# Optimization experiments

Hardware: AMD Instinct MI355X
Metric: run time of the kernel (lower is better)

Reference implementation:

```python
import jax, jax.numpy as jnp
import numpy as np

N, E = 50000, 800000
D_IN, H, D_OUT = 100, 128, 40
N_MID = 2  # num_layers(5) - 3
EPS = 1e-5


def setup_inputs() -> dict:
    key = jax.random.key(0)
    ks = iter(jax.random.split(key, 40))
    rn = lambda shape, s=0.05: jax.random.normal(next(ks), shape, dtype=jnp.float32) * s
    inp = {
        "x": jax.random.normal(next(ks), (N, D_IN), dtype=jnp.float32),
        "edge_index": jax.random.randint(next(ks), (2, E), 0, N, dtype=jnp.int64),
        "percent": 70,
        "ricci_curvature": jax.random.normal(next(ks), (E,), dtype=jnp.float32),
        # GCNConv weights/biases
        "W1": rn((D_IN, H)), "b1": jnp.zeros((H,), jnp.float32),
        "W2": rn((D_IN + H, H)), "b2": jnp.zeros((H,), jnp.float32),
        "Wm": rn((N_MID, 2 * H, H)), "bm": jnp.zeros((N_MID, H), jnp.float32),
        "Wo": rn((2 * H, D_OUT)), "bo": jnp.zeros((D_OUT,), jnp.float32),
    }
    # BatchNorm1d params + running stats (eval mode)
    def bn_params(dim, lead=()):
        return (jnp.ones(lead + (dim,), jnp.float32),            # gamma
                jnp.zeros(lead + (dim,), jnp.float32),           # beta
                rn(lead + (dim,), 0.1),                          # running mean
                1.0 + 0.1 * jax.random.uniform(next(ks), lead + (dim,), dtype=jnp.float32))  # running var
    inp["bn1_g"], inp["bn1_b"], inp["bn1_m"], inp["bn1_v"] = bn_params(D_IN)
    inp["bn2_g"], inp["bn2_b"], inp["bn2_m"], inp["bn2_v"] = bn_params(D_IN + H)
    inp["bnm_g"], inp["bnm_b"], inp["bnm_m"], inp["bnm_v"] = bn_params(2 * H, (N_MID,))
    inp["bno_g"], inp["bno_b"], inp["bno_m"], inp["bno_v"] = bn_params(2 * H)
    return inp


def reference(x, edge_index, percent, ricci_curvature,
              W1, b1, W2, b2, Wm, bm, Wo, bo,
              bn1_g, bn1_b, bn1_m, bn1_v,
              bn2_g, bn2_b, bn2_m, bn2_v,
              bnm_g, bnm_b, bnm_m, bnm_v,
              bno_g, bno_b, bno_m, bno_v):
    # Eval mode: no sampling / dynamic edge weights, dropout = identity,
    # BN uses running stats. GCNConv = PyG: add self-loops, sym-norm D^-1/2 A D^-1/2.
    n = x.shape[0]
    loop = jnp.arange(n)
    src = jnp.concatenate([edge_index[0], loop])  # [E+N]
    dst = jnp.concatenate([edge_index[1], loop])
    deg = jnp.zeros((n,), x.dtype).at[dst].add(1.0)  # >=1 thanks to self-loops
    dis = jax.lax.rsqrt(deg)
    norm = (dis[src] * dis[dst])[:, None]  # [E+N, 1]

    def gcn(h, W, b):
        hw = h @ W  # [N, out]
        agg = jnp.zeros((n, W.shape[1]), h.dtype).at[dst].add(hw[src] * norm)
        return agg + b

    def bn(h, g, bta, m, v):
        return (h - m) * (g * jax.lax.rsqrt(v + EPS)) + bta

    res = []
    x_in = x
    h = jax.nn.relu(gcn(bn(x, bn1_g, bn1_b, bn1_m, bn1_v), W1, b1))
    res.append(h)
    h = jnp.concatenate([h, x_in], axis=1)  # [N, H+D_IN]
    h = jax.nn.relu(gcn(bn(h, bn2_g, bn2_b, bn2_m, bn2_v), W2, b2))
    res.append(h)
    h = jnp.concatenate([h, res[-2]], axis=1)  # [N, 2H]
    for i in range(Wm.shape[0]):
        hi = jax.nn.relu(gcn(bn(h, bnm_g[i], bnm_b[i], bnm_m[i], bnm_v[i]), Wm[i], bm[i]))
        res.append(hi)
        h = jnp.concatenate([hi, res[-2]], axis=1)
    out = gcn(bn(h, bno_g, bno_b, bno_m, bno_v), Wo, bo)
    return (out, *res)
```

## Files before the change

### kernel.cpp

```cpp
#include <hip/hip_runtime.h>
#include <hip/hip_bf16.h>
#include <cstdint>
#include <cstddef>

#define BN_EPS 1e-5f
typedef long long ll;
using bf16x8 = __attribute__((ext_vector_type(8))) short;
using f32x4  = __attribute__((ext_vector_type(4))) float;

__device__ __forceinline__ unsigned short f2bf(float f) {
    union { float f; unsigned u; } c; c.f = f;
    unsigned u = c.u;
    u += 0x7fff + ((u >> 16) & 1);
    return (unsigned short)(u >> 16);
}
__device__ __forceinline__ float bf2f(unsigned h) {
    union { unsigned u; float f; } c; c.u = h << 16;
    return c.f;
}
__device__ __forceinline__ void addbf(float* a, uint2 v) {
    a[0] += bf2f(v.x & 0xffffu); a[1] += bf2f(v.x >> 16);
    a[2] += bf2f(v.y & 0xffffu); a[3] += bf2f(v.y >> 16);
}
__device__ __forceinline__ float4 bf4_to_f4(uint2 v) {
    return make_float4(bf2f(v.x & 0xffffu), bf2f(v.x >> 16),
                       bf2f(v.y & 0xffffu), bf2f(v.y >> 16));
}

__global__ __launch_bounds__(1024) void detect_kernel(const int* ei32, int* flag) {
    __shared__ int any;
    if (threadIdx.x == 0) any = 0;
    __syncthreads();
    for (int i = threadIdx.x; i < 2048; i += 1024) {
        if (ei32[2 * i + 1] != 0) any = 1;
    }
    __syncthreads();
    if (threadIdx.x == 0) *flag = (any == 0) ? 1 : 0;
}

__global__ void init_kernel(int* deg, int* cursor, int N) {
    int i = blockIdx.x * 256 + threadIdx.x;
    if (i < N) { deg[i] = 1; cursor[i] = 0; }
}

__global__ void count_kernel(const void* ei, int E, int* deg, const int* flag) {
    int e = blockIdx.x * 256 + threadIdx.x;
    if (e >= E) return;
    int d = (*flag) ? (int)((const ll*)ei)[(size_t)E + e]
                    : ((const int*)ei)[(size_t)E + e];
    atomicAdd(&deg[d], 1);
}

__global__ __launch_bounds__(1024) void scanA_kernel(const int* deg, int* row_ptr,
                                                     int* bsum, float* dis, int N) {
    __shared__ int wsum[16];
    int i = blockIdx.x * 1024 + threadIdx.x;
    int lane = threadIdx.x & 63, wid = threadIdx.x >> 6;
    int dv = (i < N) ? deg[i] : 1;
    if (i < N) dis[i] = rsqrtf((float)dv);
    int v = (i < N) ? (dv - 1) : 0;
    int s = v;
#pragma unroll
    for (int o = 1; o < 64; o <<= 1) { int t = __shfl_up(s, o); if (lane >= o) s += t; }
    if (lane == 63) wsum[wid] = s;
    __syncthreads();
    if (threadIdx.x < 16) {
        int w = wsum[threadIdx.x];
        int ws_ = w;
#pragma unroll
        for (int o = 1; o < 16; o <<= 1) { int t = __shfl_up(ws_, o); if ((int)threadIdx.x >= o) ws_ += t; }
        wsum[threadIdx.x] = ws_ - w;
    }
    __syncthreads();
    s += wsum[wid];
    if (i < N) row_ptr[i + 1] = s;
    if (threadIdx.x == 1023) bsum[blockIdx.x] = s;
}

__global__ void scanB_kernel(int* bsum, int nb) {
    int lane = threadIdx.x;
    int v = (lane < nb) ? bsum[lane] : 0;
    int s = v;
#pragma unroll
    for (int o = 1; o < 64; o <<= 1) { int t = __shfl_up(s, o); if (lane >= o) s += t; }
    if (lane < nb) bsum[lane] = s - v;
}

__global__ __launch_bounds__(1024) void scanC_kernel(int* row_ptr, const int* bsum, int N) {
    int i = blockIdx.x * 1024 + threadIdx.x;
    if (i < N) row_ptr[i + 1] += bsum[blockIdx.x];
    if (i == 0) row_ptr[0] = 0;
}

__global__ void fill_kernel(const void* ei, int E, const int* row_ptr,
                            int* cursor, int* csr, const int* flag) {
    int e = blockIdx.x * 256 + threadIdx.x;
    if (e >= E) return;
    int s, d;
    if (*flag) { const ll* p = (const ll*)ei; s = (int)p[e]; d = (int)p[(size_t)E + e]; }
    else       { const int* p = (const int*)ei; s = p[e]; d = p[(size_t)E + e]; }
    int pos = atomicAdd(&cursor[d], 1);
    csr[row_ptr[d] + pos] = s;
}

struct LayerP {
    const float *W, *g, *b, *m, *v;
    int K, Dout, ncb, boff;
};
struct LayerPs { LayerP l[5]; };

__global__ __launch_bounds__(256) void fold_b_all(LayerPs P,
                                                  unsigned short* __restrict__ Bhi,
                                                  unsigned short* __restrict__ Blo) {
    const LayerP& L = P.l[blockIdx.y];
    int nkc = (L.K + 63) >> 6 << 1;
    int total = nkc * L.ncb * 512;
    int idx = blockIdx.x * 256 + threadIdx.x;
    if (idx >= total) return;
    int i = idx & 7;
    int lane = (idx >> 3) & 63;
    int cb = (idx >> 9) % L.ncb;
    int kc = (idx >> 9) / L.ncb;
    int k = kc * 32 + (lane >> 4) * 8 + i;
    int col = cb * 16 + (lane & 15);
    float val = 0.f;
    if (k < L.K && col < L.Dout) {
        float s = L.g[k] * rsqrtf(L.v[k] + BN_EPS);
        val = L.W[k * L.Dout + col] * s;
    }
    unsigned short h = f2bf(val);
    Bhi[L.boff + idx] = h;
    Blo[L.boff + idx] = f2bf(val - bf2f(h));
}

__global__ __launch_bounds__(256) void fold_c_all(LayerPs P, float* __restrict__ cvecA) {
    const LayerP& L = P.l[blockIdx.y];
    int wid = threadIdx.x >> 6, lane = threadIdx.x & 63;
    int col = blockIdx.x * 4 + wid;
    float acc = 0.f;
    if (col < L.Dout) {
        for (int k = lane; k < L.K; k += 64) {
            float s = L.g[k] * rsqrtf(L.v[k] + BN_EPS);
            acc += (L.b[k] - L.m[k] * s) * L.W[k * L.Dout + col];
        }
    }
#pragma unroll
    for (int o = 32; o >= 1; o >>= 1) acc += __shfl_xor(acc, o);
    if (lane == 0 && col < 128) cvecA[128 * blockIdx.y + col] = (col < L.Dout) ? acc : 0.f;
}

template <int NCB, bool B1, bool B2>
__global__ __launch_bounds__(256, 3) void gemm_mix_kernel(
    const void* __restrict__ X1, int K1, int ld1,
    const void* __restrict__ X2, int ld2,
    const unsigned short* __restrict__ Bhi, const unsigned short* __restrict__ Blo,
    const float* __restrict__ cvec, const float* __restrict__ dis,
    unsigned short* __restrict__ outp, int ldH, int Dout, int K, int kc_lo, int N)
{
    __shared__ float Xs[64 * 64];
    const int tid = threadIdx.x;
    const int w = tid >> 6, lane = tid & 63;
    const int lr = lane & 15, lg = lane >> 4;
    const int brow = blockIdx.x * 64;
    const int nkt = (K + 63) >> 6;

    f32x4 acc[NCB];
#pragma unroll
    for (int cb = 0; cb < NCB; ++cb) {
        float cv = cvec[cb * 16 + lr];
        f32x4 iv = {cv, cv, cv, cv};
        acc[cb] = iv;
    }

    for (int kt = 0; kt < nkt; ++kt) {
        const int k0 = kt * 64;
#pragma unroll
        for (int p = 0; p < 4; ++p) {
            int fidx = (p * 256 + tid) * 4;
            int r = fidx >> 6;
            int c = fidx & 63;
            int grow = brow + r;
            int k = k0 + c;
            float4 val = make_float4(0.f, 0.f, 0.f, 0.f);
            if (grow < N) {
                if (k < K1) {
                    if (B1) val = bf4_to_f4(*(const uint2*)((const unsigned short*)X1 + (size_t)grow * ld1 + k));
                    else    val = *(const float4*)((const float*)X1 + (size_t)grow * ld1 + k);
                } else if (k < K) {
                    int kk = k - K1;
                    if (B2) val = bf4_to_f4(*(const uint2*)((const unsigned short*)X2 + (size_t)grow * ld2 + kk));
                    else    val = *(const float4*)((const float*)X2 + (size_t)grow * ld2 + kk);
                }
            }
            *(float4*)((char*)Xs + r * 256 + ((c * 4) ^ ((r & 7) << 4))) = val;
        }
        __syncthreads();

        const int r = w * 16 + lr;
        const char* base = (const char*)Xs + r * 256;
        const int swz = (r & 7) << 4;
#pragma unroll
        for (int ks = 0; ks < 2; ++ks) {
            const int kcg = kt * 2 + ks;
            const bool need_lo = (kcg >= kc_lo);
            int cb0 = ks * 128 + lg * 32;
            float4 v0 = *(const float4*)(base + (cb0 ^ swz));
            float4 v1 = *(const float4*)(base + ((cb0 + 16) ^ swz));
            float xv[8] = {v0.x, v0.y, v0.z, v0.w, v1.x, v1.y, v1.z, v1.w};
            bf16x8 ahi, alo;
#pragma unroll
            for (int i = 0; i < 8; ++i) {
                unsigned short h = f2bf(xv[i]);
                ahi[i] = (short)h;
                alo[i] = need_lo ? (short)f2bf(xv[i] - bf2f(h)) : (short)0;
            }
            const bf16x8* bh = (const bf16x8*)Bhi + (size_t)kcg * NCB * 64;
            const bf16x8* bl = (const bf16x8*)Blo + (size_t)kcg * NCB * 64;
#pragma unroll
            for (int cb = 0; cb < NCB; ++cb) {
                bf16x8 bhf = bh[cb * 64 + lane];
                bf16x8 blf = bl[cb * 64 + lane];
                acc[cb] = __builtin_amdgcn_mfma_f32_16x16x32_bf16(ahi, bhf, acc[cb], 0, 0, 0);
                acc[cb] = __builtin_amdgcn_mfma_f32_16x16x32_bf16(ahi, blf, acc[cb], 0, 0, 0);
                if (need_lo)
                    acc[cb] = __builtin_amdgcn_mfma_f32_16x16x32_bf16(alo, bhf, acc[cb], 0, 0, 0);
            }
        }
        __syncthreads();
    }

#pragma unroll
    for (int r = 0; r < 4; ++r) {
        int grow = brow + w * 16 + lg * 4 + r;
        if (grow >= N) continue;
        float d = dis[grow];
#pragma unroll
        for (int cb = 0; cb < NCB; ++cb) {
            int col = cb * 16 + lr;
            if (col < Dout) outp[(size_t)grow * ldH + col] = f2bf(d * acc[cb][r]);
        }
    }
}

template <int NCB>
__global__ __launch_bounds__(256, 4) void gemm_bf_kernel(
    const unsigned short* __restrict__ X1, int K1, int ld1,
    const unsigned short* __restrict__ X2, int ld2,
    const unsigned short* __restrict__ Bhi, const unsigned short* __restrict__ Blo,
    const float* __restrict__ cvec, const float* __restrict__ dis,
    unsigned short* __restrict__ outp, int ldH, int Dout, int K, int N)
{
    __shared__ unsigned short Xs[64 * 64];
    const int tid = threadIdx.x;
    const int w = tid >> 6, lane = tid & 63;
    const int lr = lane & 15, lg = lane >> 4;
    const int brow = blockIdx.x * 64;
    const int nkt = (K + 63) >> 6;

    f32x4 acc[NCB];
#pragma unroll
    for (int cb = 0; cb < NCB; ++cb) {
        float cv = cvec[cb * 16 + lr];
        f32x4 iv = {cv, cv, cv, cv};
        acc[cb] = iv;
    }

    for (int kt = 0; kt < nkt; ++kt) {
        const int k0 = kt * 64;
#pragma unroll
        for (int p = 0; p < 2; ++p) {
            int idx = p * 256 + tid;
            int r = idx >> 3;
            int sl = idx & 7;
            int grow = brow + r;
            int k = k0 + sl * 8;
            uint4 raw = make_uint4(0, 0, 0, 0);
            if (grow < N) {
                if (k < K1)      raw = *(const uint4*)(X1 + (size_t)grow * ld1 + k);
                else if (k < K)  raw = *(const uint4*)(X2 + (size_t)grow * ld2 + (k - K1));
            }
            *(uint4*)((char*)Xs + r * 128 + ((sl * 16) ^ ((r & 7) << 4))) = raw;
        }
        __syncthreads();

        const int r = w * 16 + lr;
        const char* base = (const char*)Xs + r * 128;
        const int swz = (r & 7) << 4;
        bf16x8 a0 = *(const bf16x8*)(base + ((lg * 16) ^ swz));
        bf16x8 a1 = *(const bf16x8*)(base + ((64 + lg * 16) ^ swz));
#pragma unroll
        for (int ks = 0; ks < 2; ++ks) {
            const int kcg = kt * 2 + ks;
            const bf16x8 af = ks ? a1 : a0;
            const bf16x8* bh = (const bf16x8*)Bhi + (size_t)kcg * NCB * 64;
            const bf16x8* bl = (const bf16x8*)Blo + (size_t)kcg * NCB * 64;
#pragma unroll
            for (int cb = 0; cb < NCB; ++cb) {
                bf16x8 bhf = bh[cb * 64 + lane];
                bf16x8 blf = bl[cb * 64 + lane];
                acc[cb] = __builtin_amdgcn_mfma_f32_16x16x32_bf16(af, bhf, acc[cb], 0, 0, 0);
                acc[cb] = __builtin_amdgcn_mfma_f32_16x16x32_bf16(af, blf, acc[cb], 0, 0, 0);
            }
        }
        __syncthreads();
    }

#pragma unroll
    for (int r = 0; r < 4; ++r) {
        int grow = brow + w * 16 + lg * 4 + r;
        if (grow >= N) continue;
        float d = dis[grow];
#pragma unroll
        for (int cb = 0; cb < NCB; ++cb) {
            int col = cb * 16 + lr;
            if (col < Dout) outp[(size_t)grow * ldH + col] = f2bf(d * acc[cb][r]);
        }
    }
}

template <bool RELU>
__global__ __launch_bounds__(256) void agg128b_kernel(
    const unsigned short* __restrict__ hwb,
    const int* __restrict__ row_ptr, const int* __restrict__ csr,
    const float* __restrict__ dis, const float* __restrict__ bias,
    float* __restrict__ outp, unsigned short* __restrict__ hbout, int N)
{
    int wid = threadIdx.x >> 6, lane = threadIdx.x & 63;
    int node = blockIdx.x * 4 + wid;
    if (node >= N) return;
    const int half = lane >> 5, q = lane & 31;
    const uint2* hw2 = (const uint2*)hwb;
    float a[4] = {0.f, 0.f, 0.f, 0.f};
    float b4[4] = {0.f, 0.f, 0.f, 0.f};
    if (half == 0) addbf(a, hw2[(size_t)node * 32 + q]);
    int beg = row_ptr[node], end = row_ptr[node + 1];
    for (int base = beg; base < end; base += 64) {
        int idx = base + lane;
        int j = (idx < end) ? csr[idx] : 0;
        int cnt = end - base; if (cnt > 64) cnt = 64;
        int fullp = cnt >> 1;
        int t = 0;
        for (; t + 4 <= fullp; t += 4) {
            int ja = __shfl(j, 2 * t     + half);
            int jb = __shfl(j, 2 * t + 2 + half);
            int jc = __shfl(j, 2 * t + 4 + half);
            int jd = __shfl(j, 2 * t + 6 + half);
            uint2 va = hw2[(size_t)ja * 32 + q];
            uint2 vb = hw2[(size_t)jb * 32 + q];
            uint2 vc = hw2[(size_t)jc * 32 + q];
            uint2 vd = hw2[(size_t)jd * 32 + q];
            addbf(a, va); addbf(b4, vb); addbf(a, vc); addbf(b4, vd);
        }
        for (; t < fullp; ++t) {
            int ja = __shfl(j, 2 * t + half);
            uint2 va = hw2[(size_t)ja * 32 + q];
            addbf(a, va);
        }
        if (cnt & 1) {
            int ja = __shfl(j, cnt - 1);
            if (half == 0) { uint2 va = hw2[(size_t)ja * 32 + q]; addbf(a, va); }
        }
    }
#pragma unroll
    for (int c = 0; c < 4; ++c) {
        a[c] += b4[c];
        a[c] += __shfl_xor(a[c], 32);
    }
    if (half == 0) {
        float d = dis[node];
        float4 bv = ((const float4*)bias)[q];
        float4 o;
        o.x = fmaf(d, a[0], bv.x);
        o.y = fmaf(d, a[1], bv.y);
        o.z = fmaf(d, a[2], bv.z);
        o.w = fmaf(d, a[3], bv.w);
        if (RELU) {
            o.x = fmaxf(o.x, 0.f); o.y = fmaxf(o.y, 0.f);
            o.z = fmaxf(o.z, 0.f); o.w = fmaxf(o.w, 0.f);
        }
        ((float4*)outp)[(size_t)node * 32 + q] = o;
        uint2 pk;
        pk.x = (unsigned)f2bf(o.x) | ((unsigned)f2bf(o.y) << 16);
        pk.y = (unsigned)f2bf(o.z) | ((unsigned)f2bf(o.w) << 16);
        ((uint2*)hbout)[(size_t)node * 32 + q] = pk;
    }
}

__global__ __launch_bounds__(256) void agg40b_kernel(
    const unsigned short* __restrict__ hwb,
    const int* __restrict__ row_ptr, const int* __restrict__ csr,
    const float* __restrict__ dis, const float* __restrict__ bias,
    float* __restrict__ outp, int N)
{
    int wid = threadIdx.x >> 6, lane = threadIdx.x & 63;
    int node = blockIdx.x * 4 + wid;
    if (node >= N) return;
    const int half = lane >> 5, q = lane & 31;
    const bool act = q < 20;
    const unsigned* hw20 = (const unsigned*)hwb;
    float a0 = 0.f, a1 = 0.f, b0 = 0.f, b1 = 0.f;
    if (half == 0 && act) {
        unsigned v = hw20[(size_t)node * 20 + q];
        a0 += bf2f(v & 0xffffu); a1 += bf2f(v >> 16);
    }
    int beg = row_ptr[node], end = row_ptr[node + 1];
    for (int base = beg; base < end; base += 64) {
        int idx = base + lane;
        int j = (idx < end) ? csr[idx] : 0;
        int cnt = end - base; if (cnt > 64) cnt = 64;
        int fullp = cnt >> 1;
        int t = 0;
        for (; t + 4 <= fullp; t += 4) {
            int ja = __shfl(j, 2 * t     + half);
            int jb = __shfl(j, 2 * t + 2 + half);
            int jc = __shfl(j, 2 * t + 4 + half);
            int jd = __shfl(j, 2 * t + 6 + half);
            if (act) {
                unsigned va = hw20[(size_t)ja * 20 + q];
                unsigned vb = hw20[(size_t)jb * 20 + q];
                unsigned vc = hw20[(size_t)jc * 20 + q];
                unsigned vd = hw20[(size_t)jd * 20 + q];
                a0 += bf2f(va & 0xffffu); a1 += bf2f(va >> 16);
                b0 += bf2f(vb & 0xffffu); b1 += bf2f(vb >> 16);
                a0 += bf2f(vc & 0xffffu); a1 += bf2f(vc >> 16);
                b0 += bf2f(vd & 0xffffu); b1 += bf2f(vd >> 16);
            }
        }
        for (; t < fullp; ++t) {
            int ja = __shfl(j, 2 * t + half);
            if (act) {
                unsigned va = hw20[(size_t)ja * 20 + q];
                a0 += bf2f(va & 0xffffu); a1 += bf2f(va >> 16);
            }
        }
        if (cnt & 1) {
            int ja = __shfl(j, cnt - 1);
            if (half == 0 && act) {
                unsigned va = hw20[(size_t)ja * 20 + q];
                a0 += bf2f(va & 0xffffu); a1 += bf2f(va >> 16);
            }
        }
    }
    a0 += b0; a1 += b1;
    a0 += __shfl_xor(a0, 32);
    a1 += __shfl_xor(a1, 32);
    if (half == 0 && act) {
        float d = dis[node];
        float2 o;
        o.x = fmaf(d, a0, bias[2 * q]);
        o.y = fmaf(d, a1, bias[2 * q + 1]);
        *(float2*)(outp + (size_t)node * 40 + 2 * q) = o;
    }
}

extern "C" void kernel_launch(void* const* d_in, const int* in_sizes, int n_in,
                              void* d_out, int out_size, void* d_ws, size_t ws_size,
                              hipStream_t stream) {
    const int N = in_sizes[0] / 100;
    const int E = in_sizes[1] / 2;

    const float* x   = (const float*)d_in[0];
    const void*  ei  = d_in[1];
    const float* W1  = (const float*)d_in[4];
    const float* b1  = (const float*)d_in[5];
    const float* W2  = (const float*)d_in[6];
    const float* b2  = (const float*)d_in[7];
    const float* Wm  = (const float*)d_in[8];
    const float* bm  = (const float*)d_in[9];
    const float* Wo  = (const float*)d_in[10];
    const float* bo  = (const float*)d_in[11];
    const float* bn1g = (const float*)d_in[12];
    const float* bn1b = (const float*)d_in[13];
    const float* bn1m = (const float*)d_in[14];
    const float* bn1v = (const float*)d_in[15];
    const float* bn2g = (const float*)d_in[16];
    const float* bn2b = (const float*)d_in[17];
    const float* bn2m = (const float*)d_in[18];
    const float* bn2v = (const float*)d_in[19];
    const float* bnmg = (const float*)d_in[20];
    const float* bnmb = (const float*)d_in[21];
    const float* bnmm = (const float*)d_in[22];
    const float* bnmv = (const float*)d_in[23];
    const float* bnog = (const float*)d_in[24];
    const float* bnob = (const float*)d_in[25];
    const float* bnom = (const float*)d_in[26];
    const float* bnov = (const float*)d_in[27];

    char* wsb = (char*)d_ws;
    size_t off = 0;
    auto alloc = [&](size_t elems) -> void* { void* p = wsb + off; off += elems * 4; return p; };
    int*   deg     = (int*)alloc(N);
    int*   cursor  = (int*)alloc(N);
    int*   row_ptr = (int*)alloc((size_t)N + 1);
    int*   bsum    = (int*)alloc(64);
    int*   flag    = (int*)alloc(1);
    off = (off + 15) & ~(size_t)15;
    float* dis  = (float*)alloc(N);
    int*   csr  = (int*)alloc(E);
    off = (off + 15) & ~(size_t)15;
    unsigned short* hwb = (unsigned short*)alloc((size_t)N * 64);
    unsigned short* hbA = (unsigned short*)alloc((size_t)N * 64);
    unsigned short* hbB = (unsigned short*)alloc((size_t)N * 64);
    unsigned short* hbC = (unsigned short*)alloc((size_t)N * 64);
    unsigned short* BhiA = (unsigned short*)alloc(63488);
    unsigned short* BloA = (unsigned short*)alloc(63488);
    float* cvecA = (float*)alloc(128 * 5);
    (void)ws_size; (void)n_in; (void)out_size;

    float* outF = (float*)d_out;
    float* h1 = outF + (size_t)N * 40;
    float* h2 = h1 + (size_t)N * 128;
    float* h3 = h2 + (size_t)N * 128;
    float* h4 = h3 + (size_t)N * 128;

    dim3 b256(256);

    LayerPs P;
    P.l[0] = {W1, bn1g, bn1b, bn1m, bn1v, 100, 128, 8, 0};
    P.l[1] = {W2, bn2g, bn2b, bn2m, bn2v, 228, 128, 8, 16384};
    P.l[2] = {Wm, bnmg, bnmb, bnmm, bnmv, 256, 128, 8, 49152};
    P.l[3] = {Wm + 256 * 128, bnmg + 256, bnmb + 256, bnmm + 256, bnmv + 256, 256, 128, 8, 81920};
    P.l[4] = {Wo, bnog, bnob, bnom, bnov, 256, 40, 3, 114688};
    fold_b_all<<<dim3(128, 5), b256, 0, stream>>>(P, BhiA, BloA);
    fold_c_all<<<dim3(32, 5), b256, 0, stream>>>(P, cvecA);

    detect_kernel<<<1, 1024, 0, stream>>>((const int*)ei, flag);
    init_kernel<<<dim3((N + 255) / 256), b256, 0, stream>>>(deg, cursor, N);
    count_kernel<<<dim3((E + 255) / 256), b256, 0, stream>>>(ei, E, deg, flag);
    int nb = (N + 1023) / 1024;
    scanA_kernel<<<dim3(nb), dim3(1024), 0, stream>>>(deg, row_ptr, bsum, dis, N);
    scanB_kernel<<<1, 64, 0, stream>>>(bsum, nb);
    scanC_kernel<<<dim3(nb), dim3(1024), 0, stream>>>(row_ptr, bsum, N);
    fill_kernel<<<dim3((E + 255) / 256), b256, 0, stream>>>(ei, E, row_ptr, cursor, csr, flag);

    int gemm_grid = (N + 63) / 64;
    int agg_grid  = (N + 3) / 4;

    auto agg128 = [&](const float* lb, float* dst, unsigned short* hbout) {
        agg128b_kernel<true><<<dim3(agg_grid), b256, 0, stream>>>(
            hwb, row_ptr, csr, dis, lb, dst, hbout, N);
    };

    gemm_mix_kernel<8, false, false><<<dim3(gemm_grid), b256, 0, stream>>>(
        x, 100, 100, nullptr, 0, BhiA + P.l[0].boff, BloA + P.l[0].boff,
        cvecA, dis, hwb, 128, 128, 100, 0, N);
    agg128(b1, h1, hbA);

    gemm_mix_kernel<8, true, false><<<dim3(gemm_grid), b256, 0, stream>>>(
        hbA, 128, 128, x, 100, BhiA + P.l[1].boff, BloA + P.l[1].boff,
        cvecA + 128, dis, hwb, 128, 128, 228, 4, N);
    agg128(b2, h2, hbB);

    gemm_bf_kernel<8><<<dim3(gemm_grid), b256, 0, stream>>>(
        hbB, 128, 128, hbA, 128, BhiA + P.l[2].boff, BloA + P.l[2].boff,
        cvecA + 256, dis, hwb, 128, 128, 256, N);
    agg128(bm, h3, hbC);

    gemm_bf_kernel<8><<<dim3(gemm_grid), b256, 0, stream>>>(
        hbC, 128, 128, hbB, 128, BhiA + P.l[3].boff, BloA + P.l[3].boff,
        cvecA + 384, dis, hwb, 128, 128, 256, N);
    agg128(bm + 128, h4, hbA);

    gemm_bf_kernel<3><<<dim3(gemm_grid), b256, 0, stream>>>(
        hbA, 128, 128, hbC, 128, BhiA + P.l[4].boff, BloA + P.l[4].boff,
        cvecA + 512, dis, hwb, 40, 40, 256, N);
    agg40b_kernel<<<dim3(agg_grid), b256, 0, stream>>>(hwb, row_ptr, csr, dis, bo, outF, N);
}
```

Baseline: 432.5 us.

## Split GEMM columns across waves, pre-convert A to bf16 in LDS, merge setup kernels

```diff
diff --git a/kernel.cpp b/kernel.cpp
--- a/kernel.cpp
+++ b/kernel.cpp
@@ -27,20 +27,18 @@
                        bf2f(v.y & 0xffffu), bf2f(v.y >> 16));
 }
 
-__global__ __launch_bounds__(1024) void detect_kernel(const int* ei32, int* flag) {
-    __shared__ int any;
-    if (threadIdx.x == 0) any = 0;
-    __syncthreads();
-    for (int i = threadIdx.x; i < 2048; i += 1024) {
-        if (ei32[2 * i + 1] != 0) any = 1;
-    }
-    __syncthreads();
-    if (threadIdx.x == 0) *flag = (any == 0) ? 1 : 0;
-}
-
-__global__ void init_kernel(int* deg, int* cursor, int N) {
+__global__ void build0_kernel(const int* ei32, int* flag, int* deg, int* cursor, int N) {
     int i = blockIdx.x * 256 + threadIdx.x;
     if (i < N) { deg[i] = 1; cursor[i] = 0; }
+    if (blockIdx.x == 0) {
+        __shared__ int any;
+        if (threadIdx.x == 0) any = 0;
+        __syncthreads();
+        for (int t = threadIdx.x; t < 2048; t += 256)
+            if (ei32[2 * t + 1] != 0) any = 1;
+        __syncthreads();
+        if (threadIdx.x == 0) *flag = (any == 0) ? 1 : 0;
+    }
 }
 
 __global__ void count_kernel(const void* ei, int E, int* deg, const int* flag) {
@@ -109,71 +107,157 @@
 };
 struct LayerPs { LayerP l[5]; };
 
-__global__ __launch_bounds__(256) void fold_b_all(LayerPs P,
-                                                  unsigned short* __restrict__ Bhi,
-                                                  unsigned short* __restrict__ Blo) {
+__global__ __launch_bounds__(256) void fold_all(LayerPs P,
+                                                unsigned short* __restrict__ Bhi,
+                                                unsigned short* __restrict__ Blo,
+                                                float* __restrict__ cvecA) {
     const LayerP& L = P.l[blockIdx.y];
-    int nkc = (L.K + 63) >> 6 << 1;
-    int total = nkc * L.ncb * 512;
-    int idx = blockIdx.x * 256 + threadIdx.x;
-    if (idx >= total) return;
-    int i = idx & 7;
-    int lane = (idx >> 3) & 63;
-    int cb = (idx >> 9) % L.ncb;
-    int kc = (idx >> 9) / L.ncb;
-    int k = kc * 32 + (lane >> 4) * 8 + i;
-    int col = cb * 16 + (lane & 15);
-    float val = 0.f;
-    if (k < L.K && col < L.Dout) {
-        float s = L.g[k] * rsqrtf(L.v[k] + BN_EPS);
-        val = L.W[k * L.Dout + col] * s;
-    }
-    unsigned short h = f2bf(val);
-    Bhi[L.boff + idx] = h;
-    Blo[L.boff + idx] = f2bf(val - bf2f(h));
-}
-
-__global__ __launch_bounds__(256) void fold_c_all(LayerPs P, float* __restrict__ cvecA) {
-    const LayerP& L = P.l[blockIdx.y];
-    int wid = threadIdx.x >> 6, lane = threadIdx.x & 63;
-    int col = blockIdx.x * 4 + wid;
-    float acc = 0.f;
-    if (col < L.Dout) {
-        for (int k = lane; k < L.K; k += 64) {
+    if (blockIdx.x < 128) {
+        int nkc = (L.K + 63) >> 6 << 1;
+        int total = nkc * L.ncb * 512;
+        int idx = blockIdx.x * 256 + threadIdx.x;
+        if (idx >= total) return;
+        int i = idx & 7;
+        int lane = (idx >> 3) & 63;
+        int cb = (idx >> 9) % L.ncb;
+        int kc = (idx >> 9) / L.ncb;
+        int k = kc * 32 + (lane >> 4) * 8 + i;
+        int col = cb * 16 + (lane & 15);
+        float val = 0.f;
+        if (k < L.K && col < L.Dout) {
             float s = L.g[k] * rsqrtf(L.v[k] + BN_EPS);
-            acc += (L.b[k] - L.m[k] * s) * L.W[k * L.Dout + col];
-        }
-    }
-#pragma unroll
-    for (int o = 32; o >= 1; o >>= 1) acc += __shfl_xor(acc, o);
-    if (lane == 0 && col < 128) cvecA[128 * blockIdx.y + col] = (col < L.Dout) ? acc : 0.f;
-}
-
-template <int NCB, bool B1, bool B2>
-__global__ __launch_bounds__(256, 3) void gemm_mix_kernel(
-    const void* __restrict__ X1, int K1, int ld1,
-    const void* __restrict__ X2, int ld2,
+            val = L.W[k * L.Dout + col] * s;
+        }
+        unsigned short h = f2bf(val);
+        Bhi[L.boff + idx] = h;
+        Blo[L.boff + idx] = f2bf(val - bf2f(h));
+    } else {
+        int wid = threadIdx.x >> 6, lane = threadIdx.x & 63;
+        int col = (blockIdx.x - 128) * 4 + wid;
+        float acc = 0.f;
+        if (col < L.Dout) {
+            for (int k = lane; k < L.K; k += 64) {
+                float s = L.g[k] * rsqrtf(L.v[k] + BN_EPS);
+                acc += (L.b[k] - L.m[k] * s) * L.W[k * L.Dout + col];
+            }
+        }
+#pragma unroll
+        for (int o = 32; o >= 1; o >>= 1) acc += __shfl_xor(acc, o);
+        if (lane == 0 && col < 128) cvecA[128 * blockIdx.y + col] = (col < L.Dout) ? acc : 0.f;
+    }
+}
+
+__global__ __launch_bounds__(256, 4) void gemm_bf2_kernel(
+    const unsigned short* __restrict__ X1, int K1, int ld1,
+    const unsigned short* __restrict__ X2, int ld2,
     const unsigned short* __restrict__ Bhi, const unsigned short* __restrict__ Blo,
     const float* __restrict__ cvec, const float* __restrict__ dis,
-    unsigned short* __restrict__ outp, int ldH, int Dout, int K, int kc_lo, int N)
+    unsigned short* __restrict__ outp, int K, int N)
 {
-    __shared__ float Xs[64 * 64];
+    __shared__ unsigned short Xs[64 * 64];
     const int tid = threadIdx.x;
     const int w = tid >> 6, lane = tid & 63;
     const int lr = lane & 15, lg = lane >> 4;
     const int brow = blockIdx.x * 64;
     const int nkt = (K + 63) >> 6;
-
-    f32x4 acc[NCB];
-#pragma unroll
-    for (int cb = 0; cb < NCB; ++cb) {
-        float cv = cvec[cb * 16 + lr];
+    const int cb0 = 2 * w;
+
+    f32x4 acc[4][2];
+#pragma unroll
+    for (int c = 0; c < 2; ++c) {
+        float cv = cvec[(cb0 + c) * 16 + lr];
         f32x4 iv = {cv, cv, cv, cv};
-        acc[cb] = iv;
+#pragma unroll
+        for (int rb = 0; rb < 4; ++rb) acc[rb][c] = iv;
     }
 
     for (int kt = 0; kt < nkt; ++kt) {
         const int k0 = kt * 64;
+#pragma unroll
+        for (int p = 0; p < 2; ++p) {
+            int idx = p * 256 + tid;
+            int r = idx >> 3;
+            int sl = idx & 7;
+            int grow = brow + r;
+            int k = k0 + sl * 8;
+            uint4 raw = make_uint4(0, 0, 0, 0);
+            if (grow < N) {
+                if (k < K1)      raw = *(const uint4*)(X1 + (size_t)grow * ld1 + k);
+                else if (k < K)  raw = *(const uint4*)(X2 + (size_t)grow * ld2 + (k - K1));
+            }
+            *(uint4*)((char*)Xs + r * 128 + ((sl * 16) ^ ((r & 7) << 4))) = raw;
+        }
+        __syncthreads();
+
+#pragma unroll
+        for (int ks = 0; ks < 2; ++ks) {
+            const int kcg = kt * 2 + ks;
+            bf16x8 a[4];
+#pragma unroll
+            for (int rb = 0; rb < 4; ++rb) {
+                int r = rb * 16 + lr;
+                a[rb] = *(const bf16x8*)((const char*)Xs + r * 128 +
+                                         ((ks * 64 + lg * 16) ^ ((r & 7) << 4)));
+            }
+            const bf16x8* bh = (const bf16x8*)Bhi + (size_t)kcg * 8 * 64;
+            const bf16x8* bl = (const bf16x8*)Blo + (size_t)kcg * 8 * 64;
+#pragma unroll
+            for (int c = 0; c < 2; ++c) {
+                bf16x8 bhf = bh[(cb0 + c) * 64 + lane];
+                bf16x8 blf = bl[(cb0 + c) * 64 + lane];
+#pragma unroll
+                for (int rb = 0; rb < 4; ++rb) {
+                    acc[rb][c] = __builtin_amdgcn_mfma_f32_16x16x32_bf16(a[rb], bhf, acc[rb][c], 0, 0, 0);
+                    acc[rb][c] = __builtin_amdgcn_mfma_f32_16x16x32_bf16(a[rb], blf, acc[rb][c], 0, 0, 0);
+                }
+            }
+        }
+        __syncthreads();
+    }
+
+#pragma unroll
+    for (int rb = 0; rb < 4; ++rb) {
+#pragma unroll
+        for (int r = 0; r < 4; ++r) {
+            int grow = brow + rb * 16 + lg * 4 + r;
+            if (grow >= N) continue;
+            float d = dis[grow];
+#pragma unroll
+            for (int c = 0; c < 2; ++c)
+                outp[(size_t)grow * 128 + (cb0 + c) * 16 + lr] = f2bf(d * acc[rb][c][r]);
+        }
+    }
+}
+
+template <bool B1, bool B2>
+__global__ __launch_bounds__(256, 3) void gemm_mix2_kernel(
+    const void* __restrict__ X1, int K1, int ld1,
+    const void* __restrict__ X2, int ld2,
+    const unsigned short* __restrict__ Bhi, const unsigned short* __restrict__ Blo,
+    const float* __restrict__ cvec, const float* __restrict__ dis,
+    unsigned short* __restrict__ outp, int K, int kc_lo, int N)
+{
+    __shared__ unsigned short Xhi[64 * 64];
+    __shared__ unsigned short Xlo[64 * 64];
+    const int tid = threadIdx.x;
+    const int w = tid >> 6, lane = tid & 63;
+    const int lr = lane & 15, lg = lane >> 4;
+    const int brow = blockIdx.x * 64;
+    const int nkt = (K + 63) >> 6;
+    const int cb0 = 2 * w;
+
+    f32x4 acc[4][2];
+#pragma unroll
+    for (int c = 0; c < 2; ++c) {
+        float cv = cvec[(cb0 + c) * 16 + lr];
+        f32x4 iv = {cv, cv, cv, cv};
+#pragma unroll
+        for (int rb = 0; rb < 4; ++rb) acc[rb][c] = iv;
+    }
+
+    for (int kt = 0; kt < nkt; ++kt) {
+        const int k0 = kt * 64;
+        const bool kt_lo = (kt * 2 + 1) >= kc_lo;
 #pragma unroll
         for (int p = 0; p < 4; ++p) {
             int fidx = (p * 256 + tid) * 4;
@@ -192,63 +276,73 @@
                     else    val = *(const float4*)((const float*)X2 + (size_t)grow * ld2 + kk);
                 }
             }
-            *(float4*)((char*)Xs + r * 256 + ((c * 4) ^ ((r & 7) << 4))) = val;
-        }
-        __syncthreads();
-
-        const int r = w * 16 + lr;
-        const char* base = (const char*)Xs + r * 256;
-        const int swz = (r & 7) << 4;
+            unsigned short h0 = f2bf(val.x), h1 = f2bf(val.y),
+                           h2 = f2bf(val.z), h3 = f2bf(val.w);
+            int b8 = c * 2;
+            int addr = r * 128 + (((b8 & 0x70) ^ ((r & 7) << 4)) | (b8 & 8));
+            *(uint2*)((char*)Xhi + addr) =
+                make_uint2((unsigned)h0 | ((unsigned)h1 << 16),
+                           (unsigned)h2 | ((unsigned)h3 << 16));
+            if (kt_lo) {
+                unsigned short l0 = f2bf(val.x - bf2f(h0)), l1 = f2bf(val.y - bf2f(h1)),
+                               l2 = f2bf(val.z - bf2f(h2)), l3 = f2bf(val.w - bf2f(h3));
+                *(uint2*)((char*)Xlo + addr) =
+                    make_uint2((unsigned)l0 | ((unsigned)l1 << 16),
+                               (unsigned)l2 | ((unsigned)l3 << 16));
+            }
+        }
+        __syncthreads();
+
 #pragma unroll
         for (int ks = 0; ks < 2; ++ks) {
             const int kcg = kt * 2 + ks;
             const bool need_lo = (kcg >= kc_lo);
-            int cb0 = ks * 128 + lg * 32;
-            float4 v0 = *(const float4*)(base + (cb0 ^ swz));
-            float4 v1 = *(const float4*)(base + ((cb0 + 16) ^ swz));
-            float xv[8] = {v0.x, v0.y, v0.z, v0.w, v1.x, v1.y, v1.z, v1.w};
-            bf16x8 ahi, alo;
-#pragma unroll
-            for (int i = 0; i < 8; ++i) {
-                unsigned short h = f2bf(xv[i]);
-                ahi[i] = (short)h;
-                alo[i] = need_lo ? (short)f2bf(xv[i] - bf2f(h)) : (short)0;
-            }
-            const bf16x8* bh = (const bf16x8*)Bhi + (size_t)kcg * NCB * 64;
-            const bf16x8* bl = (const bf16x8*)Blo + (size_t)kcg * NCB * 64;
-#pragma unroll
-            for (int cb = 0; cb < NCB; ++cb) {
-                bf16x8 bhf = bh[cb * 64 + lane];
-                bf16x8 blf = bl[cb * 64 + lane];
-                acc[cb] = __builtin_amdgcn_mfma_f32_16x16x32_bf16(ahi, bhf, acc[cb], 0, 0, 0);
-                acc[cb] = __builtin_amdgcn_mfma_f32_16x16x32_bf16(ahi, blf, acc[cb], 0, 0, 0);
-                if (need_lo)
-                    acc[cb] = __builtin_amdgcn_mfma_f32_16x16x32_bf16(alo, bhf, acc[cb], 0, 0, 0);
-            }
-        }
-        __syncthreads();
-    }
-
-#pragma unroll
-    for (int r = 0; r < 4; ++r) {
-        int grow = brow + w * 16 + lg * 4 + r;
-        if (grow >= N) continue;
-        float d = dis[grow];
-#pragma unroll
-        for (int cb = 0; cb < NCB; ++cb) {
-            int col = cb * 16 + lr;
-            if (col < Dout) outp[(size_t)grow * ldH + col] = f2bf(d * acc[cb][r]);
-        }
-    }
-}
-
-template <int NCB>
-__global__ __launch_bounds__(256, 4) void gemm_bf_kernel(
+            bf16x8 ah[4], al[4];
+#pragma unroll
+            for (int rb = 0; rb < 4; ++rb) {
+                int r = rb * 16 + lr;
+                int off = ((ks * 64 + lg * 16) ^ ((r & 7) << 4));
+                ah[rb] = *(const bf16x8*)((const char*)Xhi + r * 128 + off);
+                if (need_lo) al[rb] = *(const bf16x8*)((const char*)Xlo + r * 128 + off);
+            }
+            const bf16x8* bh = (const bf16x8*)Bhi + (size_t)kcg * 8 * 64;
+            const bf16x8* bl = (const bf16x8*)Blo + (size_t)kcg * 8 * 64;
+#pragma unroll
+            for (int c = 0; c < 2; ++c) {
+                bf16x8 bhf = bh[(cb0 + c) * 64 + lane];
+                bf16x8 blf = bl[(cb0 + c) * 64 + lane];
+#pragma unroll
+                for (int rb = 0; rb < 4; ++rb) {
+                    acc[rb][c] = __builtin_amdgcn_mfma_f32_16x16x32_bf16(ah[rb], bhf, acc[rb][c], 0, 0, 0);
+                    acc[rb][c] = __builtin_amdgcn_mfma_f32_16x16x32_bf16(ah[rb], blf, acc[rb][c], 0, 0, 0);
+                    if (need_lo)
+                        acc[rb][c] = __builtin_amdgcn_mfma_f32_16x16x32_bf16(al[rb], bhf, acc[rb][c], 0, 0, 0);
+                }
+            }
+        }
+        __syncthreads();
+    }
+
+#pragma unroll
+    for (int rb = 0; rb < 4; ++rb) {
+#pragma unroll
+        for (int r = 0; r < 4; ++r) {
+            int grow = brow + rb * 16 + lg * 4 + r;
+            if (grow >= N) continue;
+            float d = dis[grow];
+#pragma unroll
+            for (int c = 0; c < 2; ++c)
+                outp[(size_t)grow * 128 + (cb0 + c) * 16 + lr] = f2bf(d * acc[rb][c][r]);
+        }
+    }
+}
+
+__global__ __launch_bounds__(256, 4) void gemm_bf40_kernel(
     const unsigned short* __restrict__ X1, int K1, int ld1,
     const unsigned short* __restrict__ X2, int ld2,
     const unsigned short* __restrict__ Bhi, const unsigned short* __restrict__ Blo,
     const float* __restrict__ cvec, const float* __restrict__ dis,
-    unsigned short* __restrict__ outp, int ldH, int Dout, int K, int N)
+    unsigned short* __restrict__ outp, int K, int N)
 {
     __shared__ unsigned short Xs[64 * 64];
     const int tid = threadIdx.x;
@@ -257,9 +351,9 @@
     const int brow = blockIdx.x * 64;
     const int nkt = (K + 63) >> 6;
 
-    f32x4 acc[NCB];
-#pragma unroll
-    for (int cb = 0; cb < NCB; ++cb) {
+    f32x4 acc[3];
+#pragma unroll
+    for (int cb = 0; cb < 3; ++cb) {
         float cv = cvec[cb * 16 + lr];
         f32x4 iv = {cv, cv, cv, cv};
         acc[cb] = iv;
@@ -292,10 +386,10 @@
         for (int ks = 0; ks < 2; ++ks) {
             const int kcg = kt * 2 + ks;
             const bf16x8 af = ks ? a1 : a0;
-            const bf16x8* bh = (const bf16x8*)Bhi + (size_t)kcg * NCB * 64;
-            const bf16x8* bl = (const bf16x8*)Blo + (size_t)kcg * NCB * 64;
-#pragma unroll
-            for (int cb = 0; cb < NCB; ++cb) {
+            const bf16x8* bh = (const bf16x8*)Bhi + (size_t)kcg * 3 * 64;
+            const bf16x8* bl = (const bf16x8*)Blo + (size_t)kcg * 3 * 64;
+#pragma unroll
+            for (int cb = 0; cb < 3; ++cb) {
                 bf16x8 bhf = bh[cb * 64 + lane];
                 bf16x8 blf = bl[cb * 64 + lane];
                 acc[cb] = __builtin_amdgcn_mfma_f32_16x16x32_bf16(af, bhf, acc[cb], 0, 0, 0);
@@ -311,9 +405,9 @@
         if (grow >= N) continue;
         float d = dis[grow];
 #pragma unroll
-        for (int cb = 0; cb < NCB; ++cb) {
+        for (int cb = 0; cb < 3; ++cb) {
             int col = cb * 16 + lr;
-            if (col < Dout) outp[(size_t)grow * ldH + col] = f2bf(d * acc[cb][r]);
+            if (col < 40) outp[(size_t)grow * 40 + col] = f2bf(d * acc[cb][r]);
         }
     }
 }
@@ -521,11 +615,9 @@
     P.l[2] = {Wm, bnmg, bnmb, bnmm, bnmv, 256, 128, 8, 49152};
     P.l[3] = {Wm + 256 * 128, bnmg + 256, bnmb + 256, bnmm + 256, bnmv + 256, 256, 128, 8, 81920};
     P.l[4] = {Wo, bnog, bnob, bnom, bnov, 256, 40, 3, 114688};
-    fold_b_all<<<dim3(128, 5), b256, 0, stream>>>(P, BhiA, BloA);
-    fold_c_all<<<dim3(32, 5), b256, 0, stream>>>(P, cvecA);
-
-    detect_kernel<<<1, 1024, 0, stream>>>((const int*)ei, flag);
-    init_kernel<<<dim3((N + 255) / 256), b256, 0, stream>>>(deg, cursor, N);
+    fold_all<<<dim3(160, 5), b256, 0, stream>>>(P, BhiA, BloA, cvecA);
+
+    build0_kernel<<<dim3((N + 255) / 256), b256, 0, stream>>>((const int*)ei, flag, deg, cursor, N);
     count_kernel<<<dim3((E + 255) / 256), b256, 0, stream>>>(ei, E, deg, flag);
     int nb = (N + 1023) / 1024;
     scanA_kernel<<<dim3(nb), dim3(1024), 0, stream>>>(deg, row_ptr, bsum, dis, N);
@@ -541,28 +633,28 @@
             hwb, row_ptr, csr, dis, lb, dst, hbout, N);
     };
 
-    gemm_mix_kernel<8, false, false><<<dim3(gemm_grid), b256, 0, stream>>>(
+    gemm_mix2_kernel<false, false><<<dim3(gemm_grid), b256, 0, stream>>>(
         x, 100, 100, nullptr, 0, BhiA + P.l[0].boff, BloA + P.l[0].boff,
-        cvecA, dis, hwb, 128, 128, 100, 0, N);
+        cvecA, dis, hwb, 100, 0, N);
     agg128(b1, h1, hbA);
 
-    gemm_mix_kernel<8, true, false><<<dim3(gemm_grid), b256, 0, stream>>>(
+    gemm_mix2_kernel<true, false><<<dim3(gemm_grid), b256, 0, stream>>>(
         hbA, 128, 128, x, 100, BhiA + P.l[1].boff, BloA + P.l[1].boff,
-        cvecA + 128, dis, hwb, 128, 128, 228, 4, N);
+        cvecA + 128, dis, hwb, 228, 4, N);
     agg128(b2, h2, hbB);
 
-    gemm_bf_kernel<8><<<dim3(gemm_grid), b256, 0, stream>>>(
+    gemm_bf2_kernel<<<dim3(gemm_grid), b256, 0, stream>>>(
         hbB, 128, 128, hbA, 128, BhiA + P.l[2].boff, BloA + P.l[2].boff,
-        cvecA + 256, dis, hwb, 128, 128, 256, N);
+        cvecA + 256, dis, hwb, 256, N);
     agg128(bm, h3, hbC);
 
-    gemm_bf_kernel<8><<<dim3(gemm_grid), b256, 0, stream>>>(
+    gemm_bf2_kernel<<<dim3(gemm_grid), b256, 0, stream>>>(
         hbC, 128, 128, hbB, 128, BhiA + P.l[3].boff, BloA + P.l[3].boff,
-        cvecA + 384, dis, hwb, 128, 128, 256, N);
+        cvecA + 384, dis, hwb, 256, N);
     agg128(bm + 128, h4, hbA);
 
-    gemm_bf_kernel<3><<<dim3(gemm_grid), b256, 0, stream>>>(
+    gemm_bf40_kernel<<<dim3(gemm_grid), b256, 0, stream>>>(
         hbA, 128, 128, hbC, 128, BhiA + P.l[4].boff, BloA + P.l[4].boff,
-        cvecA + 512, dis, hwb, 40, 40, 256, N);
+        cvecA + 512, dis, hwb, 256, N);
     agg40b_kernel<<<dim3(agg_grid), b256, 0, stream>>>(hwb, row_ptr, csr, dis, bo, outF, N);
 }
```

Measured after the change: 382.7 us. 11.5% less time.
